# Performance work log

Measured on AMD Instinct MI355X. Metric: run time of the kernel, lower is better.

## Reference

```python
import jax, jax.numpy as jnp
from jax import lax
import numpy as np

B, T, D_IN, H = 4096, 64, 300, 3


def setup_inputs() -> dict:
    key = jax.random.key(0)
    k_x, k_len, k_wih, k_whh, k_bih, k_bhh = jax.random.split(key, 6)
    x = jax.random.normal(k_x, (B, T, D_IN), dtype=jnp.float32)
    lengths = jax.random.randint(k_len, (B,), 1, T + 1, dtype=jnp.int64)
    # PyTorch nn.RNN init: uniform(-1/sqrt(H), 1/sqrt(H))
    bound = 1.0 / np.sqrt(H)
    W_ih = jax.random.uniform(k_wih, (H, D_IN), jnp.float32, -bound, bound)
    W_hh = jax.random.uniform(k_whh, (H, H), jnp.float32, -bound, bound)
    b_ih = jax.random.uniform(k_bih, (H,), jnp.float32, -bound, bound)
    b_hh = jax.random.uniform(k_bhh, (H,), jnp.float32, -bound, bound)
    return {"x": x, "lengths": lengths, "W_ih": W_ih, "W_hh": W_hh,
            "b_ih": b_ih, "b_hh": b_hh}


def reference(x, lengths, W_ih, W_hh, b_ih, b_hh):
    # Tanh RNN over packed variable-length sequences. The packed RNN returns
    # hidden = h at step lengths[i]-1 for each sample i; we emulate packing
    # with a masked scan: h only updates while t < lengths[i].
    Bn, Tn, _ = x.shape
    # Hoist the input projection into one big GEMM: [B,T,H]
    xb = jnp.einsum('bti,hi->bth', x, W_ih) + b_ih
    mask = jnp.arange(Tn)[None, :] < lengths[:, None]  # [B,T] bool

    def step(h, inp):
        xt, m = inp  # xt: [B,H], m: [B,1]
        h_new = jnp.tanh(xt + h @ W_hh.T + b_hh)
        return jnp.where(m, h_new, h), None

    h0 = jnp.zeros((Bn, W_hh.shape[0]), dtype=x.dtype)
    h_last, _ = lax.scan(step, h0,
                         (xb.transpose(1, 0, 2), mask.T[:, :, None]))
    return h_last  # [B, H] == hidden.squeeze(0)
```

## Files before the change

### kernel.cpp

```cpp
#include <hip/hip_runtime.h>
#include <math.h>

#define B_ 4096
#define T_ 64
#define DIN_ 300
#define H_ 3

__global__ void prep_lengths_kernel(const int* __restrict__ lraw,
                                    int* __restrict__ len32, int B) {
  __shared__ int flag;
  if (threadIdx.x == 0) flag = 0;
  __syncthreads();
  int local = 0;
  int half = B >> 1;
  for (int i = threadIdx.x; i < half; i += blockDim.x)
    if (lraw[2 * i + 1] != 0) local = 1;
  if (local) atomicOr(&flag, 1);
  __syncthreads();
  int is32 = flag;
  for (int i = threadIdx.x; i < B; i += blockDim.x) {
    int v = is32 ? lraw[i] : lraw[2 * i];
    if (v < 1) v = 1;
    if (v > T_) v = T_;
    len32[i] = v;
  }
}

__global__ __launch_bounds__(256) void rnn_fwd_kernel(
    const float* __restrict__ x,
    const int* __restrict__ len,
    const float* __restrict__ W_ih,
    const float* __restrict__ W_hh,
    const float* __restrict__ b_ih,
    const float* __restrict__ b_hh,
    float* __restrict__ out) {
  const int b = blockIdx.x;
  const int tid = threadIdx.x;
  const int wave = tid >> 6;
  const int lane = tid & 63;
  const int L = len[b];

  __shared__ float xb_s[T_][4];

  const float4* W4 = reinterpret_cast<const float4*>(W_ih);
  float4 w0[H_], w1[H_];
#pragma unroll
  for (int h = 0; h < H_; ++h) {
    w0[h] = W4[h * 75 + lane];
    if (lane < 11)
      w1[h] = W4[h * 75 + 64 + lane];
    else
      w1[h] = make_float4(0.f, 0.f, 0.f, 0.f);
  }

  const float* xrow = x + (size_t)b * T_ * DIN_;
  for (int t = wave; t < L; t += 4) {
    const float4* xt4 = reinterpret_cast<const float4*>(xrow + t * DIN_);
    float4 v0 = xt4[lane];
    float4 v1 = make_float4(0.f, 0.f, 0.f, 0.f);
    if (lane < 11) v1 = xt4[64 + lane];
    float acc[H_];
#pragma unroll
    for (int h = 0; h < H_; ++h) {
      acc[h] = v0.x * w0[h].x + v0.y * w0[h].y + v0.z * w0[h].z +
               v0.w * w0[h].w + v1.x * w1[h].x + v1.y * w1[h].y +
               v1.z * w1[h].z + v1.w * w1[h].w;
    }
#pragma unroll
    for (int off = 32; off > 0; off >>= 1) {
#pragma unroll
      for (int h = 0; h < H_; ++h) acc[h] += __shfl_down(acc[h], off, 64);
    }
    if (lane == 0) {
      xb_s[t][0] = acc[0];
      xb_s[t][1] = acc[1];
      xb_s[t][2] = acc[2];
    }
  }
  __syncthreads();

  if (tid == 0) {
    const float w00 = W_hh[0], w01 = W_hh[1], w02 = W_hh[2];
    const float w10 = W_hh[3], w11 = W_hh[4], w12 = W_hh[5];
    const float w20 = W_hh[6], w21 = W_hh[7], w22 = W_hh[8];
    const float c0 = b_ih[0] + b_hh[0];
    const float c1 = b_ih[1] + b_hh[1];
    const float c2 = b_ih[2] + b_hh[2];
    float h0 = 0.f, h1 = 0.f, h2 = 0.f;
    for (int t = 0; t < L; ++t) {
      float a0 = xb_s[t][0] + c0 + w00 * h0 + w01 * h1 + w02 * h2;
      float a1 = xb_s[t][1] + c1 + w10 * h0 + w11 * h1 + w12 * h2;
      float a2 = xb_s[t][2] + c2 + w20 * h0 + w21 * h1 + w22 * h2;
      h0 = tanhf(a0);
      h1 = tanhf(a1);
      h2 = tanhf(a2);
    }
    out[b * 3 + 0] = h0;
    out[b * 3 + 1] = h1;
    out[b * 3 + 2] = h2;
  }
}

extern "C" void kernel_launch(void* const* d_in, const int* in_sizes, int n_in,
                              void* d_out, int out_size, void* d_ws,
                              size_t ws_size, hipStream_t stream) {
  const float* x = (const float*)d_in[0];
  const int* lraw = (const int*)d_in[1];
  const float* W_ih = (const float*)d_in[2];
  const float* W_hh = (const float*)d_in[3];
  const float* b_ih = (const float*)d_in[4];
  const float* b_hh = (const float*)d_in[5];
  float* out = (float*)d_out;
  int* len32 = (int*)d_ws;

  prep_lengths_kernel<<<1, 256, 0, stream>>>(lraw, len32, B_);
  rnn_fwd_kernel<<<B_, 256, 0, stream>>>(x, len32, W_ih, W_hh, b_ih, b_hh,
                                         out);
}
```

Before: 425.2 us.

## Split projection and recurrence into separate kernels with per-sample parallel tail

```diff
diff --git a/kernel.cpp b/kernel.cpp
--- a/kernel.cpp
+++ b/kernel.cpp
@@ -5,6 +5,9 @@
 #define T_ 64
 #define DIN_ 300
 #define H_ 3
+#define NF4 75
+
+#define XB_OFF 65536
 
 __global__ void prep_lengths_kernel(const int* __restrict__ lraw,
                                     int* __restrict__ len32, int B) {
@@ -26,79 +29,96 @@
   }
 }
 
-__global__ __launch_bounds__(256) void rnn_fwd_kernel(
+__global__ __launch_bounds__(256) void proj_kernel(
     const float* __restrict__ x,
     const int* __restrict__ len,
     const float* __restrict__ W_ih,
-    const float* __restrict__ W_hh,
-    const float* __restrict__ b_ih,
-    const float* __restrict__ b_hh,
-    float* __restrict__ out) {
+    float* __restrict__ xb) {
   const int b = blockIdx.x;
   const int tid = threadIdx.x;
+
+  __shared__ float4 Wl[H_][76];
+  if (tid < H_ * NF4) {
+    int h = tid / NF4;
+    int i = tid - h * NF4;
+    Wl[h][i] = reinterpret_cast<const float4*>(W_ih)[h * NF4 + i];
+  }
+  const int L = len[b];
+  __syncthreads();
+
   const int wave = tid >> 6;
   const int lane = tid & 63;
-  const int L = len[b];
+  const int g = lane >> 2;
+  const int s = lane & 3;
+  const int row = wave * 16 + g;
+  if (wave * 16 >= L) return;
 
-  __shared__ float xb_s[T_][4];
+  const bool rowok = (row < L);
+  const float4* xr = reinterpret_cast<const float4*>(
+      x + (size_t)b * (T_ * DIN_) + (size_t)row * DIN_);
 
-  const float4* W4 = reinterpret_cast<const float4*>(W_ih);
-  float4 w0[H_], w1[H_];
-#pragma unroll
-  for (int h = 0; h < H_; ++h) {
-    w0[h] = W4[h * 75 + lane];
-    if (lane < 11)
-      w1[h] = W4[h * 75 + 64 + lane];
-    else
-      w1[h] = make_float4(0.f, 0.f, 0.f, 0.f);
-  }
-
-  const float* xrow = x + (size_t)b * T_ * DIN_;
-  for (int t = wave; t < L; t += 4) {
-    const float4* xt4 = reinterpret_cast<const float4*>(xrow + t * DIN_);
-    float4 v0 = xt4[lane];
-    float4 v1 = make_float4(0.f, 0.f, 0.f, 0.f);
-    if (lane < 11) v1 = xt4[64 + lane];
-    float acc[H_];
-#pragma unroll
-    for (int h = 0; h < H_; ++h) {
-      acc[h] = v0.x * w0[h].x + v0.y * w0[h].y + v0.z * w0[h].z +
-               v0.w * w0[h].w + v1.x * w1[h].x + v1.y * w1[h].y +
-               v1.z * w1[h].z + v1.w * w1[h].w;
-    }
-#pragma unroll
-    for (int off = 32; off > 0; off >>= 1) {
-#pragma unroll
-      for (int h = 0; h < H_; ++h) acc[h] += __shfl_down(acc[h], off, 64);
-    }
-    if (lane == 0) {
-      xb_s[t][0] = acc[0];
-      xb_s[t][1] = acc[1];
-      xb_s[t][2] = acc[2];
+  float a0 = 0.f, a1 = 0.f, a2 = 0.f;
+#pragma unroll 4
+  for (int k = 0; k < 19; ++k) {
+    int idx = 4 * k + s;
+    if (rowok && idx < NF4) {
+      float4 v = xr[idx];
+      float4 w0 = Wl[0][idx];
+      float4 w1 = Wl[1][idx];
+      float4 w2 = Wl[2][idx];
+      a0 += v.x * w0.x + v.y * w0.y + v.z * w0.z + v.w * w0.w;
+      a1 += v.x * w1.x + v.y * w1.y + v.z * w1.z + v.w * w1.w;
+      a2 += v.x * w2.x + v.y * w2.y + v.z * w2.z + v.w * w2.w;
     }
   }
-  __syncthreads();
+  a0 += __shfl_xor(a0, 1);
+  a1 += __shfl_xor(a1, 1);
+  a2 += __shfl_xor(a2, 1);
+  a0 += __shfl_xor(a0, 2);
+  a1 += __shfl_xor(a1, 2);
+  a2 += __shfl_xor(a2, 2);
 
-  if (tid == 0) {
-    const float w00 = W_hh[0], w01 = W_hh[1], w02 = W_hh[2];
-    const float w10 = W_hh[3], w11 = W_hh[4], w12 = W_hh[5];
-    const float w20 = W_hh[6], w21 = W_hh[7], w22 = W_hh[8];
-    const float c0 = b_ih[0] + b_hh[0];
-    const float c1 = b_ih[1] + b_hh[1];
-    const float c2 = b_ih[2] + b_hh[2];
-    float h0 = 0.f, h1 = 0.f, h2 = 0.f;
-    for (int t = 0; t < L; ++t) {
-      float a0 = xb_s[t][0] + c0 + w00 * h0 + w01 * h1 + w02 * h2;
-      float a1 = xb_s[t][1] + c1 + w10 * h0 + w11 * h1 + w12 * h2;
-      float a2 = xb_s[t][2] + c2 + w20 * h0 + w21 * h1 + w22 * h2;
-      h0 = tanhf(a0);
-      h1 = tanhf(a1);
-      h2 = tanhf(a2);
-    }
-    out[b * 3 + 0] = h0;
-    out[b * 3 + 1] = h1;
-    out[b * 3 + 2] = h2;
+  if (s == 0 && rowok) {
+    float* o = xb + ((size_t)row * B_ + b) * H_;
+    o[0] = a0;
+    o[1] = a1;
+    o[2] = a2;
   }
+}
+
+__device__ __forceinline__ float fast_tanh(float x) {
+  float xc = fminf(fmaxf(x, -9.0f), 9.0f);
+  float t = __expf(2.0f * xc);
+  return (t - 1.0f) * __builtin_amdgcn_rcpf(t + 1.0f);
+}
+
+__global__ __launch_bounds__(256) void tail_kernel(
+    const int* __restrict__ len, const float* __restrict__ xb,
+    const float* __restrict__ W_hh, const float* __restrict__ b_ih,
+    const float* __restrict__ b_hh, float* __restrict__ out) {
+  const int b = blockIdx.x * blockDim.x + threadIdx.x;
+  if (b >= B_) return;
+  const float w00 = W_hh[0], w01 = W_hh[1], w02 = W_hh[2];
+  const float w10 = W_hh[3], w11 = W_hh[4], w12 = W_hh[5];
+  const float w20 = W_hh[6], w21 = W_hh[7], w22 = W_hh[8];
+  const float c0 = b_ih[0] + b_hh[0];
+  const float c1 = b_ih[1] + b_hh[1];
+  const float c2 = b_ih[2] + b_hh[2];
+  const int L = len[b];
+  float h0 = 0.f, h1 = 0.f, h2 = 0.f;
+  const float* p = xb + (size_t)b * H_;
+  for (int t = 0; t < L; ++t) {
+    const float* q = p + (size_t)t * (B_ * H_);
+    float a0 = q[0] + c0 + w00 * h0 + w01 * h1 + w02 * h2;
+    float a1 = q[1] + c1 + w10 * h0 + w11 * h1 + w12 * h2;
+    float a2 = q[2] + c2 + w20 * h0 + w21 * h1 + w22 * h2;
+    h0 = fast_tanh(a0);
+    h1 = fast_tanh(a1);
+    h2 = fast_tanh(a2);
+  }
+  out[b * 3 + 0] = h0;
+  out[b * 3 + 1] = h1;
+  out[b * 3 + 2] = h2;
 }
 
 extern "C" void kernel_launch(void* const* d_in, const int* in_sizes, int n_in,
@@ -111,9 +131,12 @@
   const float* b_ih = (const float*)d_in[4];
   const float* b_hh = (const float*)d_in[5];
   float* out = (float*)d_out;
+
   int* len32 = (int*)d_ws;
+  float* xb = (float*)((char*)d_ws + XB_OFF);
 
   prep_lengths_kernel<<<1, 256, 0, stream>>>(lraw, len32, B_);
-  rnn_fwd_kernel<<<B_, 256, 0, stream>>>(x, len32, W_ih, W_hh, b_ih, b_hh,
-                                         out);
+  proj_kernel<<<B_, 256, 0, stream>>>(x, len32, W_ih, xb);
+  tail_kernel<<<(B_ + 255) / 256, 256, 0, stream>>>(len32, xb, W_hh, b_ih,
+                                                    b_hh, out);
 }
```

Measured after the change: 440.0 us. 3.5% more time.
